# Kernel tuning notes

Measured on AMD Instinct MI355X. Metric: run time of the kernel, lower is better.

## Reference

```python
import jax, jax.numpy as jnp
import numpy as np

NB_CAT = 8192       # nb_category per column
RANK = 16           # low-rank factor dimension
N_COLS = 4          # number of categorical columns (len(embedding_sizes))
N_PAIRS = 1048576   # number of (x, y) index pairs
FRAC_DIAG = 0.9     # fraction_diagonal init


def setup_inputs() -> dict:
    key = jax.random.key(0)
    k1, k2, k3, k4 = jax.random.split(key, 4)
    x = jax.random.randint(k1, (N_PAIRS, N_COLS), 0, NB_CAT, dtype=jnp.int32)
    y = jax.random.randint(k2, (N_PAIRS, N_COLS), 0, NB_CAT, dtype=jnp.int32)
    # params initialized as in the torch module, plus small noise so values are non-degenerate
    std = (FRAC_DIAG * jnp.ones((N_COLS, NB_CAT), dtype=jnp.float32)
           + 0.01 * jax.random.normal(k3, (N_COLS, NB_CAT), dtype=jnp.float32))
    covar_factor = ((1.0 - FRAC_DIAG) / np.float32(np.sqrt(RANK))
                    * jnp.ones((N_COLS, NB_CAT, RANK), dtype=jnp.float32)
                    + 0.01 * jax.random.normal(k4, (N_COLS, NB_CAT, RANK), dtype=jnp.float32))
    return {"x": x, "y": y, "covar_factor": covar_factor, "std": std}


def reference(x, y, covar_factor, std):
    # Build full covariance per column: F @ F.T + diag(std^2)   -> [C, N, N]
    cov = jnp.einsum('cnr,cmr->cnm', covar_factor, covar_factor)
    diag_idx = jnp.arange(cov.shape[1])
    cov = cov.at[:, diag_idx, diag_idx].add(std * std)
    # Gather requested (x, y) entries per column, then reduce (should_reduce=True)
    cols = jnp.arange(cov.shape[0])  # [C]
    vals = cov[cols[None, :], x, y]  # [B, C]
    return vals.sum(axis=-1)         # [B]
```

## Files before the change

kernel.cpp:

```cpp
#include <hip/hip_runtime.h>

#define NB_CAT  8192
#define RANK    16
#define N_COLS  4
#define N_PAIRS 1048576

#define NSLICE      16
#define SLICE_ROWS  NB_CAT
#define SLICE_BYTES (SLICE_ROWS * 8)
#define TBL_BYTES   ((size_t)NSLICE * SLICE_BYTES)
#define LDS_BYTES   (2 * SLICE_BYTES)
#define PART_BYTES  ((size_t)N_PAIRS * 4)
#define WS_NEED     (TBL_BYTES + 2 * PART_BYTES)

typedef _Float16 half2_t __attribute__((ext_vector_type(2)));

#if defined(__has_builtin)
#if __has_builtin(__builtin_amdgcn_fdot2)
#define HAVE_FDOT2 1
#endif
#endif

__device__ __forceinline__ float dot4_f16(uint2 A, uint2 B, float acc) {
#ifdef HAVE_FDOT2
    acc = __builtin_amdgcn_fdot2(__builtin_bit_cast(half2_t, A.x), __builtin_bit_cast(half2_t, B.x), acc, false);
    acc = __builtin_amdgcn_fdot2(__builtin_bit_cast(half2_t, A.y), __builtin_bit_cast(half2_t, B.y), acc, false);
#else
    half2_t ax = __builtin_bit_cast(half2_t, A.x), bx = __builtin_bit_cast(half2_t, B.x);
    half2_t ay = __builtin_bit_cast(half2_t, A.y), by = __builtin_bit_cast(half2_t, B.y);
    acc = fmaf((float)ax[0], (float)bx[0], acc); acc = fmaf((float)ax[1], (float)bx[1], acc);
    acc = fmaf((float)ay[0], (float)by[0], acc); acc = fmaf((float)ay[1], (float)by[1], acc);
#endif
    return acc;
}

__global__ __launch_bounds__(256) void pack_f16_kernel(
    const float4* __restrict__ src, uint2* __restrict__ dst)
{
    const int g = blockIdx.x * 256 + threadIdx.x;
    const int s = g >> 13;
    const int k = g & (NB_CAT - 1);
    const int c = s >> 2, qr = s & 3;

    const float4 f = src[(c * NB_CAT + k) * 4 + qr];
    half2_t p0 = {(_Float16)f.x, (_Float16)f.y};
    half2_t p1 = {(_Float16)f.z, (_Float16)f.w};
    uint2 u;
    u.x = __builtin_bit_cast(unsigned int, p0);
    u.y = __builtin_bit_cast(unsigned int, p1);
    dst[g] = u;
}

__global__ __launch_bounds__(1024, 1) void IndexKernel_32238024524411_kernel(
    const int2*  __restrict__ x2,
    const int2*  __restrict__ y2,
    const uint2* __restrict__ tbl,
    const float* __restrict__ stdv,
    float*       __restrict__ part)
{
    extern __shared__ uint2 sh[];

    const int tid   = threadIdx.x;
    const int g     = blockIdx.x >> 7;
    const int chunk = blockIdx.x & 127;
    const int base  = chunk * 8192 + tid;

    const uint2* gtbl = tbl + (size_t)(g * 8) * SLICE_ROWS;

    int2 xi[8], yi[8];
#pragma unroll
    for (int j = 0; j < 8; ++j) {
        const size_t p = (size_t)(base + j * 1024);
        xi[j] = x2[p * 2 + g];
        yi[j] = y2[p * 2 + g];
    }

    float acc[8] = {0.f, 0.f, 0.f, 0.f, 0.f, 0.f, 0.f, 0.f};

    const float* sd0 = stdv + (size_t)(2 * g) * NB_CAT;
    const float* sd1 = stdv + (size_t)(2 * g + 1) * NB_CAT;
#pragma unroll
    for (int j = 0; j < 8; ++j) {
        if (xi[j].x == yi[j].x) { const float s = sd0[xi[j].x]; acc[j] = fmaf(s, s, acc[j]); }
        if (xi[j].y == yi[j].y) { const float s = sd1[xi[j].y]; acc[j] = fmaf(s, s, acc[j]); }
    }

    uint2 stg[8];
#pragma unroll
    for (int it = 0; it < 8; ++it) stg[it] = gtbl[tid + it * 1024];

#define PHASE(S)                                                               \
    {                                                                          \
        constexpr int s  = (S);                                                \
        constexpr int cl = s >> 2;                          \
        uint2* buf = sh + (s & 1) * SLICE_ROWS;                                \
        _Pragma("unroll")                                                      \
        for (int it = 0; it < 8; ++it) buf[tid + it * 1024] = stg[it];         \
        if (s < 7) {                                                           \
            const uint2* nsrc = gtbl + (size_t)(s + 1) * SLICE_ROWS;           \
            _Pragma("unroll")                                                  \
            for (int it = 0; it < 8; ++it) stg[it] = nsrc[tid + it * 1024];    \
        }                                                                      \
              \
        asm volatile("s_waitcnt lgkmcnt(0)" ::: "memory");                     \
        __builtin_amdgcn_s_barrier();                                          \
        asm volatile("" ::: "memory");                                         \
        _Pragma("unroll")                                                      \
        for (int j = 0; j < 8; ++j) {                                          \
            const int a = cl ? xi[j].y : xi[j].x;                              \
            const int b = cl ? yi[j].y : yi[j].x;                              \
            acc[j] = dot4_f16(buf[a], buf[b], acc[j]);                         \
        }                                                                      \
        asm volatile("" ::: "memory");                                         \
    }

    PHASE(0) PHASE(1) PHASE(2) PHASE(3)
    PHASE(4) PHASE(5) PHASE(6) PHASE(7)
#undef PHASE

    float* my = part + (size_t)g * N_PAIRS;
#pragma unroll
    for (int j = 0; j < 8; ++j) {
        my[base + j * 1024] = acc[j];
    }
}

__global__ __launch_bounds__(256) void reduce_kernel(
    const float4* __restrict__ p0, const float4* __restrict__ p1,
    float4* __restrict__ out)
{
    const int i = blockIdx.x * 256 + threadIdx.x;
    const float4 a = p0[i];
    const float4 b = p1[i];
    out[i] = float4{a.x + b.x, a.y + b.y, a.z + b.z, a.w + b.w};
}

__global__ __launch_bounds__(256) void fallback_kernel(
    const int* __restrict__ x, const int* __restrict__ y,
    const float4* __restrict__ cf, const float* __restrict__ stdv,
    float* __restrict__ out)
{
    const int tid = threadIdx.x;
    const int q = tid & 15, gi = tid >> 4, c = q >> 2, s = q & 3;
    const int p0 = blockIdx.x * 32 + gi, p1 = p0 + 16;
    const int rb = c * NB_CAT;
    const int xi0 = x[p0*4+c], yi0 = y[p0*4+c], xi1 = x[p1*4+c], yi1 = y[p1*4+c];
    const float4 a0 = cf[(size_t)(rb+xi0)*4 + s], b0 = cf[(size_t)(rb+yi0)*4 + s];
    const float4 a1 = cf[(size_t)(rb+xi1)*4 + s], b1 = cf[(size_t)(rb+yi1)*4 + s];
    float v0 = a0.x*b0.x; v0 = fmaf(a0.y,b0.y,v0); v0 = fmaf(a0.z,b0.z,v0); v0 = fmaf(a0.w,b0.w,v0);
    float v1 = a1.x*b1.x; v1 = fmaf(a1.y,b1.y,v1); v1 = fmaf(a1.z,b1.z,v1); v1 = fmaf(a1.w,b1.w,v1);
    if (s == 0 && xi0 == yi0) { float sd = stdv[rb+xi0]; v0 = fmaf(sd,sd,v0); }
    if (s == 0 && xi1 == yi1) { float sd = stdv[rb+yi1]; v1 = fmaf(sd,sd,v1); }
    int t;
    t = __builtin_amdgcn_update_dpp(0, __float_as_int(v0), 0xB1, 0xF, 0xF, true); v0 += __int_as_float(t);
    t = __builtin_amdgcn_update_dpp(0, __float_as_int(v0), 0x4E, 0xF, 0xF, true); v0 += __int_as_float(t);
    t = __builtin_amdgcn_update_dpp(0, __float_as_int(v0), 0x141,0xF, 0xF, true); v0 += __int_as_float(t);
    t = __builtin_amdgcn_update_dpp(0, __float_as_int(v0), 0x128,0xF, 0xF, true); v0 += __int_as_float(t);
    t = __builtin_amdgcn_update_dpp(0, __float_as_int(v1), 0xB1, 0xF, 0xF, true); v1 += __int_as_float(t);
    t = __builtin_amdgcn_update_dpp(0, __float_as_int(v1), 0x4E, 0xF, 0xF, true); v1 += __int_as_float(t);
    t = __builtin_amdgcn_update_dpp(0, __float_as_int(v1), 0x141,0xF, 0xF, true); v1 += __int_as_float(t);
    t = __builtin_amdgcn_update_dpp(0, __float_as_int(v1), 0x128,0xF, 0xF, true); v1 += __int_as_float(t);
    if (q == 0) { out[p0] = v0; out[p1] = v1; }
}

extern "C" void kernel_launch(void* const* d_in, const int* in_sizes, int n_in,
                              void* d_out, int out_size, void* d_ws, size_t ws_size,
                              hipStream_t stream) {
    const int*   x    = (const int*)d_in[0];
    const int*   y    = (const int*)d_in[1];
    const float* cf   = (const float*)d_in[2];
    const float* stdv = (const float*)d_in[3];
    float*       out  = (float*)d_out;

    if (ws_size < WS_NEED) {
        fallback_kernel<<<N_PAIRS / 32, 256, 0, stream>>>(
            x, y, (const float4*)cf, stdv, out);
        return;
    }

    (void)hipFuncSetAttribute(
        reinterpret_cast<const void*>(&IndexKernel_32238024524411_kernel),
        hipFuncAttributeMaxDynamicSharedMemorySize, LDS_BYTES);

    uint2* tbl   = (uint2*)d_ws;
    float* part  = (float*)((char*)d_ws + TBL_BYTES);

    pack_f16_kernel<<<NSLICE * NB_CAT / 256, 256, 0, stream>>>(
        (const float4*)cf, tbl);

    IndexKernel_32238024524411_kernel<<<256, 1024, LDS_BYTES, stream>>>(
        (const int2*)x, (const int2*)y, tbl, stdv, part);

    reduce_kernel<<<N_PAIRS / 4 / 256, 256, 0, stream>>>(
        (const float4*)part, (const float4*)(part + N_PAIRS), (float4*)out);
}
```

Before: 95.89 us.

## Widen LDS table slices to 8 halves and single-buffer with fewer phases

Repacks the fp16 factor table into 16-byte slices of 8 rank elements, so each phase does one 128-bit LDS gather per index and runs a dot8, halving the phase count from 8 to 4. The double-buffered LDS is replaced by one 128KB buffer. The next slice is prefetched into registers during compute and written after an extra barrier. This cuts per-phase barrier and gather overhead but serialises the LDS write behind compute, adds a second barrier per phase, and raises register pressure. The fallback kernel's stdv index is also switched to xi1, which gives the same value because that branch only runs when xi1 equals yi1.

```diff
diff --git a/kernel.cpp b/kernel.cpp
--- a/kernel.cpp
+++ b/kernel.cpp
@@ -5,11 +5,11 @@
 #define N_COLS  4
 #define N_PAIRS 1048576
 
-#define NSLICE      16
+#define NSLICE      8
 #define SLICE_ROWS  NB_CAT
-#define SLICE_BYTES (SLICE_ROWS * 8)
+#define SLICE_BYTES (SLICE_ROWS * 16)
 #define TBL_BYTES   ((size_t)NSLICE * SLICE_BYTES)
-#define LDS_BYTES   (2 * SLICE_BYTES)
+#define LDS_BYTES   SLICE_BYTES
 #define PART_BYTES  ((size_t)N_PAIRS * 4)
 #define WS_NEED     (TBL_BYTES + 2 * PART_BYTES)
 
@@ -21,51 +21,64 @@
 #endif
 #endif
 
-__device__ __forceinline__ float dot4_f16(uint2 A, uint2 B, float acc) {
+__device__ __forceinline__ float dot8_f16(uint4 A, uint4 B, float acc) {
 #ifdef HAVE_FDOT2
     acc = __builtin_amdgcn_fdot2(__builtin_bit_cast(half2_t, A.x), __builtin_bit_cast(half2_t, B.x), acc, false);
     acc = __builtin_amdgcn_fdot2(__builtin_bit_cast(half2_t, A.y), __builtin_bit_cast(half2_t, B.y), acc, false);
+    acc = __builtin_amdgcn_fdot2(__builtin_bit_cast(half2_t, A.z), __builtin_bit_cast(half2_t, B.z), acc, false);
+    acc = __builtin_amdgcn_fdot2(__builtin_bit_cast(half2_t, A.w), __builtin_bit_cast(half2_t, B.w), acc, false);
 #else
     half2_t ax = __builtin_bit_cast(half2_t, A.x), bx = __builtin_bit_cast(half2_t, B.x);
     half2_t ay = __builtin_bit_cast(half2_t, A.y), by = __builtin_bit_cast(half2_t, B.y);
+    half2_t az = __builtin_bit_cast(half2_t, A.z), bz = __builtin_bit_cast(half2_t, B.z);
+    half2_t aw = __builtin_bit_cast(half2_t, A.w), bw = __builtin_bit_cast(half2_t, B.w);
     acc = fmaf((float)ax[0], (float)bx[0], acc); acc = fmaf((float)ax[1], (float)bx[1], acc);
     acc = fmaf((float)ay[0], (float)by[0], acc); acc = fmaf((float)ay[1], (float)by[1], acc);
+    acc = fmaf((float)az[0], (float)bz[0], acc); acc = fmaf((float)az[1], (float)bz[1], acc);
+    acc = fmaf((float)aw[0], (float)bw[0], acc); acc = fmaf((float)aw[1], (float)bw[1], acc);
 #endif
     return acc;
 }
 
 __global__ __launch_bounds__(256) void pack_f16_kernel(
-    const float4* __restrict__ src, uint2* __restrict__ dst)
+    const float4* __restrict__ src, uint4* __restrict__ dst)
 {
     const int g = blockIdx.x * 256 + threadIdx.x;
     const int s = g >> 13;
     const int k = g & (NB_CAT - 1);
-    const int c = s >> 2, qr = s & 3;
-
-    const float4 f = src[(c * NB_CAT + k) * 4 + qr];
-    half2_t p0 = {(_Float16)f.x, (_Float16)f.y};
-    half2_t p1 = {(_Float16)f.z, (_Float16)f.w};
-    uint2 u;
+    const int c = s >> 1, h = s & 1;
+
+    const float4 f0 = src[(c * NB_CAT + k) * 4 + h * 2];
+    const float4 f1 = src[(c * NB_CAT + k) * 4 + h * 2 + 1];
+
+    half2_t p0 = {(_Float16)f0.x, (_Float16)f0.y};
+    half2_t p1 = {(_Float16)f0.z, (_Float16)f0.w};
+    half2_t p2 = {(_Float16)f1.x, (_Float16)f1.y};
+    half2_t p3 = {(_Float16)f1.z, (_Float16)f1.w};
+
+    uint4 u;
     u.x = __builtin_bit_cast(unsigned int, p0);
     u.y = __builtin_bit_cast(unsigned int, p1);
+    u.z = __builtin_bit_cast(unsigned int, p2);
+    u.w = __builtin_bit_cast(unsigned int, p3);
     dst[g] = u;
 }
 
 __global__ __launch_bounds__(1024, 1) void IndexKernel_32238024524411_kernel(
     const int2*  __restrict__ x2,
     const int2*  __restrict__ y2,
-    const uint2* __restrict__ tbl,
+    const uint4* __restrict__ tbl,
     const float* __restrict__ stdv,
     float*       __restrict__ part)
 {
-    extern __shared__ uint2 sh[];
+    extern __shared__ uint4 sh[];
 
     const int tid   = threadIdx.x;
     const int g     = blockIdx.x >> 7;
     const int chunk = blockIdx.x & 127;
     const int base  = chunk * 8192 + tid;
 
-    const uint2* gtbl = tbl + (size_t)(g * 8) * SLICE_ROWS;
+    const uint4* gtbl = tbl + (size_t)(g * 4) * SLICE_ROWS;
 
     int2 xi[8], yi[8];
 #pragma unroll
@@ -85,37 +98,47 @@
         if (xi[j].y == yi[j].y) { const float s = sd1[xi[j].y]; acc[j] = fmaf(s, s, acc[j]); }
     }
 
-    uint2 stg[8];
-#pragma unroll
-    for (int it = 0; it < 8; ++it) stg[it] = gtbl[tid + it * 1024];
+#pragma unroll
+    for (int it = 0; it < 8; ++it) sh[tid + it * 1024] = gtbl[tid + it * 1024];
+    asm volatile("s_waitcnt lgkmcnt(0)" ::: "memory");
+    __builtin_amdgcn_s_barrier();
+    asm volatile("" ::: "memory");
+
+    uint4 t0, t1, t2, t3, t4, t5, t6, t7;
 
 #define PHASE(S)                                                               \
     {                                                                          \
         constexpr int s  = (S);                                                \
-        constexpr int cl = s >> 2;                          \
-        uint2* buf = sh + (s & 1) * SLICE_ROWS;                                \
-        _Pragma("unroll")                                                      \
-        for (int it = 0; it < 8; ++it) buf[tid + it * 1024] = stg[it];         \
-        if (s < 7) {                                                           \
-            const uint2* nsrc = gtbl + (size_t)(s + 1) * SLICE_ROWS;           \
-            _Pragma("unroll")                                                  \
-            for (int it = 0; it < 8; ++it) stg[it] = nsrc[tid + it * 1024];    \
+        constexpr int cl = s >> 1;                          \
+        if (s < 3) {                                                           \
+            const uint4* nsrc = gtbl + (size_t)(s + 1) * SLICE_ROWS;           \
+            t0 = nsrc[tid];             t1 = nsrc[tid + 1024];                 \
+            t2 = nsrc[tid + 2 * 1024];  t3 = nsrc[tid + 3 * 1024];             \
+            t4 = nsrc[tid + 4 * 1024];  t5 = nsrc[tid + 5 * 1024];             \
+            t6 = nsrc[tid + 6 * 1024];  t7 = nsrc[tid + 7 * 1024];             \
         }                                                                      \
-              \
-        asm volatile("s_waitcnt lgkmcnt(0)" ::: "memory");                     \
-        __builtin_amdgcn_s_barrier();                                          \
         asm volatile("" ::: "memory");                                         \
         _Pragma("unroll")                                                      \
         for (int j = 0; j < 8; ++j) {                                          \
             const int a = cl ? xi[j].y : xi[j].x;                              \
             const int b = cl ? yi[j].y : yi[j].x;                              \
-            acc[j] = dot4_f16(buf[a], buf[b], acc[j]);                         \
+            acc[j] = dot8_f16(sh[a], sh[b], acc[j]);                           \
         }                                                                      \
-        asm volatile("" ::: "memory");                                         \
+        if (s < 3) {                                                           \
+            asm volatile("s_waitcnt lgkmcnt(0)" ::: "memory");                 \
+            __builtin_amdgcn_s_barrier();                                      \
+            asm volatile("" ::: "memory");                                     \
+            sh[tid]            = t0;  sh[tid + 1024]     = t1;                 \
+            sh[tid + 2 * 1024] = t2;  sh[tid + 3 * 1024] = t3;                 \
+            sh[tid + 4 * 1024] = t4;  sh[tid + 5 * 1024] = t5;                 \
+            sh[tid + 6 * 1024] = t6;  sh[tid + 7 * 1024] = t7;                 \
+            asm volatile("s_waitcnt lgkmcnt(0)" ::: "memory");                 \
+            __builtin_amdgcn_s_barrier();                                      \
+            asm volatile("" ::: "memory");                                     \
+        }                                                                      \
     }
 
     PHASE(0) PHASE(1) PHASE(2) PHASE(3)
-    PHASE(4) PHASE(5) PHASE(6) PHASE(7)
 #undef PHASE
 
     float* my = part + (size_t)g * N_PAIRS;
@@ -150,7 +173,7 @@
     float v0 = a0.x*b0.x; v0 = fmaf(a0.y,b0.y,v0); v0 = fmaf(a0.z,b0.z,v0); v0 = fmaf(a0.w,b0.w,v0);
     float v1 = a1.x*b1.x; v1 = fmaf(a1.y,b1.y,v1); v1 = fmaf(a1.z,b1.z,v1); v1 = fmaf(a1.w,b1.w,v1);
     if (s == 0 && xi0 == yi0) { float sd = stdv[rb+xi0]; v0 = fmaf(sd,sd,v0); }
-    if (s == 0 && xi1 == yi1) { float sd = stdv[rb+yi1]; v1 = fmaf(sd,sd,v1); }
+    if (s == 0 && xi1 == yi1) { float sd = stdv[rb+xi1]; v1 = fmaf(sd,sd,v1); }
     int t;
     t = __builtin_amdgcn_update_dpp(0, __float_as_int(v0), 0xB1, 0xF, 0xF, true); v0 += __int_as_float(t);
     t = __builtin_amdgcn_update_dpp(0, __float_as_int(v0), 0x4E, 0xF, 0xF, true); v0 += __int_as_float(t);
@@ -182,8 +205,8 @@
         reinterpret_cast<const void*>(&IndexKernel_32238024524411_kernel),
         hipFuncAttributeMaxDynamicSharedMemorySize, LDS_BYTES);
 
-    uint2* tbl   = (uint2*)d_ws;
-    float* part  = (float*)((char*)d_ws + TBL_BYTES);
+    uint4* tbl  = (uint4*)d_ws;
+    float* part = (float*)((char*)d_ws + TBL_BYTES);
 
     pack_f16_kernel<<<NSLICE * NB_CAT / 256, 256, 0, stream>>>(
         (const float4*)cf, tbl);
```

New measurement: 94.12 us. About the same (-1.8%).
